# Performance work log

Hardware: AMD Instinct MI355X
Metric: run time of the kernel (lower is better)

Reference implementation:

```python
import jax, jax.numpy as jnp
import numpy as np

B, NB, DIM = 4096, 64, 256
CNT_R = 500
CNT_E = CNT_R * 2  # padding relation id == CNT_E maps to the masked row
N_WR = CNT_R * 2 + 1
N_ZQ = CNT_R * 2


def setup_inputs() -> dict:
    key = jax.random.key(0)
    ks = jax.random.split(key, 10)
    batch_nei_rid = jax.random.randint(ks[0], (B, NB), 0, N_WR, dtype=jnp.int64 if jax.config.read('jax_enable_x64') else jnp.int32)
    batch_nei_e_emb = jax.random.normal(ks[1], (B, NB, DIM), dtype=jnp.float32)
    batch_nei_rw = jax.random.uniform(ks[2], (B, NB), dtype=jnp.float32)
    batch_q_rid = jax.random.randint(ks[3], (B,), 0, N_ZQ, dtype=jnp.int32)
    # xavier-normal-ish params
    def xav(k, shape):
        fan_in, fan_out = shape[-1], shape[-2] if len(shape) > 1 else shape[-1]
        std = (2.0 / (fan_in + fan_out)) ** 0.5
        return (jax.random.normal(k, shape) * std).astype(jnp.float32)
    w_r_weight = xav(ks[4], (N_WR, DIM))
    zq_weight = xav(ks[5], (N_ZQ, DIM))
    attn_W_w = xav(ks[6], (2 * DIM, 2 * DIM))   # [out, in], torch Linear layout
    attn_W_b = jnp.zeros((2 * DIM,), jnp.float32)
    u_a_w = xav(ks[7], (1, 2 * DIM))
    u_a_b = jnp.zeros((1,), jnp.float32)
    return {
        'batch_nei_rid': batch_nei_rid,
        'batch_nei_e_emb': batch_nei_e_emb,
        'batch_nei_rw': batch_nei_rw,
        'batch_q_rid': batch_q_rid,
        'w_r_weight': w_r_weight,
        'zq_weight': zq_weight,
        'attn_W_w': attn_W_w,
        'attn_W_b': attn_W_b,
        'u_a_w': u_a_w,
        'u_a_b': u_a_b,
    }


def reference(batch_nei_rid, batch_nei_e_emb, batch_nei_rw, batch_q_rid,
              w_r_weight, zq_weight, attn_W_w, attn_W_b, u_a_w, u_a_b):
    # relation hyperplane gather + TransH-style projection
    w_r = w_r_weight[batch_nei_rid]                                   # [B,NB,D]
    nrm = jnp.maximum(jnp.linalg.norm(w_r, axis=-1, keepdims=True), 1e-12)
    wn = w_r / nrm                                                    # f.normalize(p=2)
    e_tr = batch_nei_e_emb - jnp.sum(batch_nei_e_emb * wn, axis=-1, keepdims=True) * wn
    # mask_emb: 1 for real rows, 0 for padding row (index CNT_E)
    mask = (batch_nei_rid < CNT_E).astype(e_tr.dtype)[..., None]
    e_tr = e_tr * mask
    # nn attention: concat(z_q, e_Tr) -> Linear -> tanh -> Linear(1)
    z_q = zq_weight[batch_q_rid][:, None, :]                          # [B,1,D]
    cat = jnp.concatenate([jnp.broadcast_to(z_q, e_tr.shape), e_tr], axis=-1)  # [B,NB,2D]
    h = jnp.tanh(jnp.einsum('bni,oi->bno', cat, attn_W_w) + attn_W_b)
    _alpha = jnp.einsum('bni,oi->bno', h, u_a_w)[..., 0] + u_a_b[0]   # [B,NB]
    # mask_weight: 1e19 at padding row, subtracted before softmax
    _alpha = _alpha - jnp.where(batch_nei_rid == CNT_E, jnp.asarray(1e19, _alpha.dtype), jnp.asarray(0.0, _alpha.dtype))
    alpha = jax.nn.softmax(_alpha, axis=-1)
    attn = alpha + batch_nei_rw                                       # use_logic_attention
    return jnp.sum(attn[..., None] * e_tr, axis=-2)                   # [B,D]
```

## Files before the change

### kernel.cpp

```cpp
#include <hip/hip_runtime.h>
#include <math.h>

#define NB    64
#define DIM   256
#define TWOD  512
#define CNTE  1000
#define E2S   264
#define NQ    1000

typedef __attribute__((ext_vector_type(8))) short short8;
typedef __attribute__((ext_vector_type(4))) float f32x4;

union U16x8 { uint4 u; short8 s; };

__device__ __forceinline__ unsigned short f2bf(float x) {
    unsigned int u = __float_as_uint(x);
    u += 0x7fffu + ((u >> 16) & 1u);
    return (unsigned short)(u >> 16);
}
__device__ __forceinline__ float bf2f(unsigned short h) {
    return __uint_as_float(((unsigned int)h) << 16);
}

__global__ __launch_bounds__(128) void zpre_kernel(
    const float* __restrict__ zq_w, const float* __restrict__ attn_W,
    const float* __restrict__ attn_b, float* __restrict__ zpre)
{
    __shared__ float zq[8][DIM];
    const int t  = threadIdx.x;
    const int q0 = blockIdx.x * 8;
    const int o  = blockIdx.y * 128 + t;
    #pragma unroll
    for (int r = 0; r < 8; ++r) {
        zq[r][t]       = zq_w[(size_t)(q0 + r) * DIM + t];
        zq[r][t + 128] = zq_w[(size_t)(q0 + r) * DIM + t + 128];
    }
    __syncthreads();
    const float4* wrow = (const float4*)(attn_W + (size_t)o * TWOD);
    float acc[8];
    #pragma unroll
    for (int r = 0; r < 8; ++r) acc[r] = 0.f;
    #pragma unroll 8
    for (int kk = 0; kk < 64; ++kk) {
        float4 w = wrow[kk];
        #pragma unroll
        for (int r = 0; r < 8; ++r)
            acc[r] += w.x * zq[r][kk * 4 + 0] + w.y * zq[r][kk * 4 + 1]
                    + w.z * zq[r][kk * 4 + 2] + w.w * zq[r][kk * 4 + 3];
    }
    const float bo = attn_b[o];
    #pragma unroll
    for (int r = 0; r < 8; ++r)
        zpre[(size_t)(q0 + r) * TWOD + o] = acc[r] + bo;
}

__global__ __launch_bounds__(256) void pack_w_kernel(
    const float* __restrict__ attn_W, unsigned short* __restrict__ wbf)
{
    int f = blockIdx.x * 256 + threadIdx.x;
    int j    = f & 7;
    int lane = (f >> 3) & 63;
    int kt   = (f >> 9) & 7;
    int ot   = f >> 12;
    int o  = ot * 16 + (lane & 15);
    int ke = kt * 32 + (lane >> 4) * 8 + j;
    wbf[f] = f2bf(attn_W[(size_t)o * TWOD + 256 + ke]);
}

__global__ __launch_bounds__(256, 2) void encoder_attn_kernel(
    const int*   __restrict__ nei_rid,
    const float* __restrict__ nei_e,
    const float* __restrict__ nei_rw,
    const int*   __restrict__ q_rid,
    const float* __restrict__ w_r,
    const float* __restrict__ zq_w,
    const float* __restrict__ attn_W,
    const float* __restrict__ attn_b,
    const float* __restrict__ u_a_w,
    const float* __restrict__ zpre,
    const unsigned short* __restrict__ wbf,
    float*       __restrict__ out,
    int has_zpre)
{
    __shared__ __align__(16) unsigned short e2[NB * E2S];
    __shared__ float2 zu[TWOD];
    __shared__ __align__(16) float red_a[256];
    __shared__ float  pen[NB];
    __shared__ float  attn_lds[NB];

    const int b = blockIdx.x;
    const int t = threadIdx.x;
    const int qr = q_rid[b];

    if (has_zpre) {
        zu[t]       = make_float2(zpre[(size_t)qr * TWOD + t],       u_a_w[t]);
        zu[t + 256] = make_float2(zpre[(size_t)qr * TWOD + t + 256], u_a_w[t + 256]);
    } else {
        red_a[t] = zq_w[(size_t)qr * DIM + t];
        __syncthreads();
        float a0 = 0.f, a1 = 0.f;
        const float4* w0 = (const float4*)(attn_W + (size_t)t * TWOD);
        const float4* w1 = (const float4*)(attn_W + (size_t)(t + 256) * TWOD);
        const float4* zz = (const float4*)red_a;
        #pragma unroll 8
        for (int kk = 0; kk < 64; ++kk) {
            float4 z = zz[kk], u0 = w0[kk], u1 = w1[kk];
            a0 += u0.x * z.x + u0.y * z.y + u0.z * z.z + u0.w * z.w;
            a1 += u1.x * z.x + u1.y * z.y + u1.z * z.z + u1.w * z.w;
        }
        zu[t]       = make_float2(a0 + attn_b[t],       u_a_w[t]);
        zu[t + 256] = make_float2(a1 + attn_b[t + 256], u_a_w[t + 256]);
        __syncthreads();
    }

    {
        const int n = t >> 2, q = t & 3;
        const int rid = nei_rid[b * NB + n];
        const float4* e4 = (const float4*)(nei_e + ((size_t)(b * NB + n)) * DIM) + q * 16;
        const float4* w4 = (const float4*)(w_r + (size_t)rid * DIM) + q * 16;
        float4 ev[16], wv[16];
        float sew = 0.f, sww = 0.f;
        #pragma unroll
        for (int j = 0; j < 16; ++j) {
            ev[j] = e4[j]; wv[j] = w4[j];
            sew += ev[j].x * wv[j].x + ev[j].y * wv[j].y + ev[j].z * wv[j].z + ev[j].w * wv[j].w;
            sww += wv[j].x * wv[j].x + wv[j].y * wv[j].y + wv[j].z * wv[j].z + wv[j].w * wv[j].w;
        }
        sew += __shfl_xor(sew, 1); sew += __shfl_xor(sew, 2);
        sww += __shfl_xor(sww, 1); sww += __shfl_xor(sww, 2);
        float nc   = fmaxf(sqrtf(sww), 1e-12f);
        float coef = sew / (nc * nc);
        float maskf = (rid < CNTE) ? 1.f : 0.f;
        if (q == 0) pen[n] = (rid == CNTE) ? 1e19f : 0.f;
        unsigned short* e2row = e2 + n * E2S + q * 64;
        #pragma unroll
        for (int jj = 0; jj < 8; ++jj) {
            float4 e0 = ev[jj * 2],     w0 = wv[jj * 2];
            float4 e1 = ev[jj * 2 + 1], w1 = wv[jj * 2 + 1];
            uint4 pk;
            pk.x = (unsigned int)f2bf((e0.x - coef * w0.x) * maskf)
                 | ((unsigned int)f2bf((e0.y - coef * w0.y) * maskf) << 16);
            pk.y = (unsigned int)f2bf((e0.z - coef * w0.z) * maskf)
                 | ((unsigned int)f2bf((e0.w - coef * w0.w) * maskf) << 16);
            pk.z = (unsigned int)f2bf((e1.x - coef * w1.x) * maskf)
                 | ((unsigned int)f2bf((e1.y - coef * w1.y) * maskf) << 16);
            pk.w = (unsigned int)f2bf((e1.z - coef * w1.z) * maskf)
                 | ((unsigned int)f2bf((e1.w - coef * w1.w) * maskf) << 16);
            *(uint4*)(e2row + jj * 8) = pk;
        }
    }
    __syncthreads();

    const int wv_id = t >> 6;
    const int lane  = t & 63;
    const int l15 = lane & 15, lq = lane >> 4;

    short8 afrag[4][8];
    #pragma unroll
    for (int mt = 0; mt < 4; ++mt)
        #pragma unroll
        for (int kt = 0; kt < 8; ++kt) {
            U16x8 u; u.u = *(const uint4*)(e2 + (mt * 16 + l15) * E2S + kt * 32 + lq * 8);
            afrag[mt][kt] = u.s;
        }

    f32x4 lpv[4];
    #pragma unroll
    for (int mt = 0; mt < 4; ++mt) lpv[mt] = (f32x4){0.f, 0.f, 0.f, 0.f};

    const uint4* wbase = (const uint4*)wbf + (size_t)(wv_id * 8) * 512 + lane;

    uint4 bufA[8], bufB[8];
    #pragma unroll
    for (int kt = 0; kt < 8; ++kt) bufA[kt] = wbase[kt * 64];

#define PROC_OT(OT, CUR, NXT, NOT)                                              \
    {                                                                           \
        _Pragma("unroll")                                                       \
        for (int kt = 0; kt < 8; ++kt) NXT[kt] = wbase[(NOT) * 512 + kt * 64];  \
        const int otg = wv_id * 8 + (OT);                                       \
        const float2 zub = zu[otg * 16 + l15];                                  \
        f32x4 acc[4];                                                           \
        _Pragma("unroll")                                                       \
        for (int mt = 0; mt < 4; ++mt)                                          \
            acc[mt] = (f32x4){zub.x, zub.x, zub.x, zub.x};                      \
        _Pragma("unroll")                                                       \
        for (int kt = 0; kt < 8; ++kt) {                                        \
            U16x8 u; u.u = CUR[kt];                                             \
            _Pragma("unroll")                                                   \
            for (int mt = 0; mt < 4; ++mt)                                      \
                acc[mt] = __builtin_amdgcn_mfma_f32_16x16x32_bf16(              \
                              afrag[mt][kt], u.s, acc[mt], 0, 0, 0);            \
        }                                                                       \
        const float uy2 = -2.0f * zub.y;                                        \
        _Pragma("unroll")                                                       \
        for (int mt = 0; mt < 4; ++mt)                                          \
            _Pragma("unroll")                                                   \
            for (int r = 0; r < 4; ++r) {                                       \
                float x = acc[mt][r];                                           \
                float e = __expf(x + x);                                        \
                lpv[mt][r] += uy2 * __builtin_amdgcn_rcpf(e + 1.0f);            \
            }                                                                   \
    }

    #pragma unroll 1
    for (int i = 0; i < 4; ++i) {
        PROC_OT(2 * i,     bufA, bufB, 2 * i + 1)
        PROC_OT(2 * i + 1, bufB, bufA, (2 * i + 2) & 7)
    }
#undef PROC_OT

    #pragma unroll
    for (int mt = 0; mt < 4; ++mt)
        #pragma unroll
        for (int r = 0; r < 4; ++r) {
            float v = lpv[mt][r];
            v += __shfl_xor(v, 1); v += __shfl_xor(v, 2);
            v += __shfl_xor(v, 4); v += __shfl_xor(v, 8);
            if (l15 == 0) red_a[wv_id * 64 + mt * 16 + lq * 4 + r] = v;
        }
    __syncthreads();

    if (t < NB) {
        float lgt = red_a[t] + red_a[64 + t] + red_a[128 + t] + red_a[192 + t]
                  - pen[t];
        float m = lgt;
        #pragma unroll
        for (int off = 32; off > 0; off >>= 1) m = fmaxf(m, __shfl_xor(m, off));
        float ex = __expf(lgt - m);
        float s = ex;
        #pragma unroll
        for (int off = 32; off > 0; off >>= 1) s += __shfl_xor(s, off);
        attn_lds[t] = ex / s + nei_rw[b * NB + t];
    }
    __syncthreads();

    float oacc = 0.f;
    #pragma unroll 8
    for (int nn = 0; nn < NB; ++nn)
        oacc += attn_lds[nn] * bf2f(e2[nn * E2S + t]);
    out[(size_t)b * DIM + t] = oacc;
}

extern "C" void kernel_launch(void* const* d_in, const int* in_sizes, int n_in,
                              void* d_out, int out_size, void* d_ws, size_t ws_size,
                              hipStream_t stream) {
    const int*   nei_rid = (const int*)  d_in[0];
    const float* nei_e   = (const float*)d_in[1];
    const float* nei_rw  = (const float*)d_in[2];
    const int*   q_rid   = (const int*)  d_in[3];
    const float* w_r     = (const float*)d_in[4];
    const float* zq_w    = (const float*)d_in[5];
    const float* attn_W  = (const float*)d_in[6];
    const float* attn_b  = (const float*)d_in[7];
    const float* u_a_w   = (const float*)d_in[8];

    float* out = (float*)d_out;
    const int B = in_sizes[3];

    const size_t ZPRE_BYTES = (size_t)NQ * TWOD * 4;
    const size_t WBF_BYTES  = (size_t)512 * 256 * 2;
    const int has_zpre = (ws_size >= ZPRE_BYTES + WBF_BYTES) ? 1 : 0;

    float*          zpre = (float*)d_ws;
    unsigned short* wbf  = has_zpre
        ? (unsigned short*)((char*)d_ws + ZPRE_BYTES)
        : (unsigned short*)d_ws;

    if (has_zpre)
        hipLaunchKernelGGL(zpre_kernel, dim3(NQ / 8, 4), dim3(128), 0, stream,
                           zq_w, attn_W, attn_b, zpre);
    hipLaunchKernelGGL(pack_w_kernel, dim3(512), dim3(256), 0, stream, attn_W, wbf);
    hipLaunchKernelGGL(encoder_attn_kernel, dim3(B), dim3(256), 0, stream,
                       nei_rid, nei_e, nei_rw, q_rid, w_r, zq_w, attn_W, attn_b,
                       u_a_w, zpre, wbf, out, has_zpre);
}
```

Baseline: 543.1 us.

## Split TransH projection into a separate kernel writing bf16 intermediates

Adds a standalone kernel that computes the TransH projection and masking for every neighbour row and stores the result as bf16 in workspace. A second kernel then loads these precomputed rows and runs the MFMA attention GEMM, softmax and weighted sum. The aim is to decouple the gather-heavy projection from the matrix-core stage so each can run with better occupancy. The cost is an extra round-trip of the intermediate through global memory, and the path only runs when the workspace is large enough.

```diff
diff --git a/kernel.cpp b/kernel.cpp
--- a/kernel.cpp
+++ b/kernel.cpp
@@ -65,6 +65,177 @@
     int o  = ot * 16 + (lane & 15);
     int ke = kt * 32 + (lane >> 4) * 8 + j;
     wbf[f] = f2bf(attn_W[(size_t)o * TWOD + 256 + ke]);
+}
+
+__global__ __launch_bounds__(256) void transh_kernel(
+    const int*   __restrict__ nei_rid,
+    const float* __restrict__ nei_e,
+    const float* __restrict__ w_r,
+    unsigned short* __restrict__ etr)
+{
+    const int t    = threadIdx.x;
+    const int b    = blockIdx.x >> 1;
+    const int n    = (blockIdx.x & 1) * 32 + (t >> 3);
+    const int q    = t & 7;
+    const size_t row = (size_t)b * NB + n;
+    const int rid  = nei_rid[row];
+    const float4* e4 = (const float4*)(nei_e + row * DIM) + q * 8;
+    const float4* w4 = (const float4*)(w_r + (size_t)rid * DIM) + q * 8;
+    float4 ev[8], wv[8];
+    float sew = 0.f, sww = 0.f;
+    #pragma unroll
+    for (int j = 0; j < 8; ++j) {
+        ev[j] = e4[j]; wv[j] = w4[j];
+        sew += ev[j].x * wv[j].x + ev[j].y * wv[j].y + ev[j].z * wv[j].z + ev[j].w * wv[j].w;
+        sww += wv[j].x * wv[j].x + wv[j].y * wv[j].y + wv[j].z * wv[j].z + wv[j].w * wv[j].w;
+    }
+    sew += __shfl_xor(sew, 1); sew += __shfl_xor(sew, 2); sew += __shfl_xor(sew, 4);
+    sww += __shfl_xor(sww, 1); sww += __shfl_xor(sww, 2); sww += __shfl_xor(sww, 4);
+    float nc   = fmaxf(sqrtf(sww), 1e-12f);
+    float coef = sew / (nc * nc);
+    float maskf = (rid < CNTE) ? 1.f : 0.f;
+    uint4* orow = (uint4*)(etr + row * DIM) + q * 4;
+    #pragma unroll
+    for (int jj = 0; jj < 4; ++jj) {
+        float4 e0 = ev[jj * 2],     w0 = wv[jj * 2];
+        float4 e1 = ev[jj * 2 + 1], w1 = wv[jj * 2 + 1];
+        uint4 pk;
+        pk.x = (unsigned int)f2bf((e0.x - coef * w0.x) * maskf)
+             | ((unsigned int)f2bf((e0.y - coef * w0.y) * maskf) << 16);
+        pk.y = (unsigned int)f2bf((e0.z - coef * w0.z) * maskf)
+             | ((unsigned int)f2bf((e0.w - coef * w0.w) * maskf) << 16);
+        pk.z = (unsigned int)f2bf((e1.x - coef * w1.x) * maskf)
+             | ((unsigned int)f2bf((e1.y - coef * w1.y) * maskf) << 16);
+        pk.w = (unsigned int)f2bf((e1.z - coef * w1.z) * maskf)
+             | ((unsigned int)f2bf((e1.w - coef * w1.w) * maskf) << 16);
+        orow[jj] = pk;
+    }
+}
+
+__global__ __launch_bounds__(256, 2) void encoder_gemm_kernel(
+    const int*   __restrict__ nei_rid,
+    const float* __restrict__ nei_rw,
+    const int*   __restrict__ q_rid,
+    const float* __restrict__ u_a_w,
+    const float* __restrict__ zpre,
+    const unsigned short* __restrict__ wbf,
+    const unsigned short* __restrict__ etr,
+    float*       __restrict__ out)
+{
+    __shared__ __align__(16) unsigned short e2[NB * E2S];
+    __shared__ float2 zu[TWOD];
+    __shared__ __align__(16) float red_a[256];
+    __shared__ float  pen[NB];
+    __shared__ float  attn_lds[NB];
+
+    const int b = blockIdx.x;
+    const int t = threadIdx.x;
+    const int qr = q_rid[b];
+
+    zu[t]       = make_float2(zpre[(size_t)qr * TWOD + t],       u_a_w[t]);
+    zu[t + 256] = make_float2(zpre[(size_t)qr * TWOD + t + 256], u_a_w[t + 256]);
+    if (t < NB) pen[t] = (nei_rid[b * NB + t] == CNTE) ? 1e19f : 0.f;
+
+    {
+        const uint4* src = (const uint4*)(etr + (size_t)b * NB * DIM);
+        #pragma unroll
+        for (int i = 0; i < 8; ++i) {
+            int idx = t + i * 256;
+            int row = idx >> 5, col = idx & 31;
+            *(uint4*)(e2 + row * E2S + col * 8) = src[idx];
+        }
+    }
+    __syncthreads();
+
+    const int wv_id = t >> 6;
+    const int lane  = t & 63;
+    const int l15 = lane & 15, lq = lane >> 4;
+
+    short8 afrag[4][8];
+    #pragma unroll
+    for (int mt = 0; mt < 4; ++mt)
+        #pragma unroll
+        for (int kt = 0; kt < 8; ++kt) {
+            U16x8 u; u.u = *(const uint4*)(e2 + (mt * 16 + l15) * E2S + kt * 32 + lq * 8);
+            afrag[mt][kt] = u.s;
+        }
+
+    f32x4 lpv[4];
+    #pragma unroll
+    for (int mt = 0; mt < 4; ++mt) lpv[mt] = (f32x4){0.f, 0.f, 0.f, 0.f};
+
+    const uint4* wbase = (const uint4*)wbf + (size_t)(wv_id * 8) * 512 + lane;
+
+    uint4 bufA[8], bufB[8];
+    #pragma unroll
+    for (int kt = 0; kt < 8; ++kt) bufA[kt] = wbase[kt * 64];
+
+#define PROC_OT(OT, CUR, NXT, NOT)                                              \
+    {                                                                           \
+        _Pragma("unroll")                                                       \
+        for (int kt = 0; kt < 8; ++kt) NXT[kt] = wbase[(NOT) * 512 + kt * 64];  \
+        const int otg = wv_id * 8 + (OT);                                       \
+        const float2 zub = zu[otg * 16 + l15];                                  \
+        f32x4 acc[4];                                                           \
+        _Pragma("unroll")                                                       \
+        for (int mt = 0; mt < 4; ++mt)                                          \
+            acc[mt] = (f32x4){zub.x, zub.x, zub.x, zub.x};                      \
+        _Pragma("unroll")                                                       \
+        for (int kt = 0; kt < 8; ++kt) {                                        \
+            U16x8 u; u.u = CUR[kt];                                             \
+            _Pragma("unroll")                                                   \
+            for (int mt = 0; mt < 4; ++mt)                                      \
+                acc[mt] = __builtin_amdgcn_mfma_f32_16x16x32_bf16(              \
+                              afrag[mt][kt], u.s, acc[mt], 0, 0, 0);            \
+        }                                                                       \
+        const float uy2 = -2.0f * zub.y;                                        \
+        _Pragma("unroll")                                                       \
+        for (int mt = 0; mt < 4; ++mt)                                          \
+            _Pragma("unroll")                                                   \
+            for (int r = 0; r < 4; ++r) {                                       \
+                float x = acc[mt][r];                                           \
+                float e = __expf(x + x);                                        \
+                lpv[mt][r] += uy2 * __builtin_amdgcn_rcpf(e + 1.0f);            \
+            }                                                                   \
+    }
+
+    #pragma unroll 1
+    for (int i = 0; i < 4; ++i) {
+        PROC_OT(2 * i,     bufA, bufB, 2 * i + 1)
+        PROC_OT(2 * i + 1, bufB, bufA, (2 * i + 2) & 7)
+    }
+#undef PROC_OT
+
+    #pragma unroll
+    for (int mt = 0; mt < 4; ++mt)
+        #pragma unroll
+        for (int r = 0; r < 4; ++r) {
+            float v = lpv[mt][r];
+            v += __shfl_xor(v, 1); v += __shfl_xor(v, 2);
+            v += __shfl_xor(v, 4); v += __shfl_xor(v, 8);
+            if (l15 == 0) red_a[wv_id * 64 + mt * 16 + lq * 4 + r] = v;
+        }
+    __syncthreads();
+
+    if (t < NB) {
+        float lgt = red_a[t] + red_a[64 + t] + red_a[128 + t] + red_a[192 + t]
+                  - pen[t];
+        float m = lgt;
+        #pragma unroll
+        for (int off = 32; off > 0; off >>= 1) m = fmaxf(m, __shfl_xor(m, off));
+        float ex = __expf(lgt - m);
+        float s = ex;
+        #pragma unroll
+        for (int off = 32; off > 0; off >>= 1) s += __shfl_xor(s, off);
+        attn_lds[t] = ex / s + nei_rw[b * NB + t];
+    }
+    __syncthreads();
+
+    float oacc = 0.f;
+    #pragma unroll 8
+    for (int nn = 0; nn < NB; ++nn)
+        oacc += attn_lds[nn] * bf2f(e2[nn * E2S + t]);
+    out[(size_t)b * DIM + t] = oacc;
 }
 
 __global__ __launch_bounds__(256, 2) void encoder_attn_kernel(
@@ -260,18 +431,38 @@
 
     const size_t ZPRE_BYTES = (size_t)NQ * TWOD * 4;
     const size_t WBF_BYTES  = (size_t)512 * 256 * 2;
-    const int has_zpre = (ws_size >= ZPRE_BYTES + WBF_BYTES) ? 1 : 0;
+    const size_t ETR_BYTES  = (size_t)B * NB * DIM * 2;
 
     float*          zpre = (float*)d_ws;
-    unsigned short* wbf  = has_zpre
-        ? (unsigned short*)((char*)d_ws + ZPRE_BYTES)
-        : (unsigned short*)d_ws;
-
-    if (has_zpre)
+    unsigned short* wbf;
+    unsigned short* etr = nullptr;
+
+    int mode;
+    if (ws_size >= ZPRE_BYTES + WBF_BYTES + ETR_BYTES) {
+        mode = 2;
+        wbf = (unsigned short*)((char*)d_ws + ZPRE_BYTES);
+        etr = (unsigned short*)((char*)d_ws + ZPRE_BYTES + WBF_BYTES);
+    } else if (ws_size >= ZPRE_BYTES + WBF_BYTES) {
+        mode = 1;
+        wbf = (unsigned short*)((char*)d_ws + ZPRE_BYTES);
+    } else {
+        mode = 0;
+        wbf = (unsigned short*)d_ws;
+    }
+
+    if (mode >= 1)
         hipLaunchKernelGGL(zpre_kernel, dim3(NQ / 8, 4), dim3(128), 0, stream,
                            zq_w, attn_W, attn_b, zpre);
     hipLaunchKernelGGL(pack_w_kernel, dim3(512), dim3(256), 0, stream, attn_W, wbf);
-    hipLaunchKernelGGL(encoder_attn_kernel, dim3(B), dim3(256), 0, stream,
-                       nei_rid, nei_e, nei_rw, q_rid, w_r, zq_w, attn_W, attn_b,
-                       u_a_w, zpre, wbf, out, has_zpre);
-}
+
+    if (mode == 2) {
+        hipLaunchKernelGGL(transh_kernel, dim3(B * 2), dim3(256), 0, stream,
+                           nei_rid, nei_e, w_r, etr);
+        hipLaunchKernelGGL(encoder_gemm_kernel, dim3(B), dim3(256), 0, stream,
+                           nei_rid, nei_rw, q_rid, u_a_w, zpre, wbf, etr, out);
+    } else {
+        hipLaunchKernelGGL(encoder_attn_kernel, dim3(B), dim3(256), 0, stream,
+                           nei_rid, nei_e, nei_rw, q_rid, w_r, zq_w, attn_W, attn_b,
+                           u_a_w, zpre, wbf, out, mode);
+    }
+}
```

Result: no change. 553.4 us (+1.9%).
